# Kernel tuning notes

Measured on AMD Instinct MI355X. Metric: run time of the kernel, lower is better.

## Reference

```python
import jax, jax.numpy as jnp
import numpy as np

N_NODES = 100000
N_EDGES = 1600000
IN_DIM = 256
OUT_DIM = 128


def setup_inputs() -> dict:
    key = jax.random.key(0)
    k1, k2, k3, k4 = jax.random.split(key, 4)
    x = jax.random.normal(k1, (N_NODES, IN_DIM), dtype=jnp.float32)
    edge_list = jax.random.randint(k2, (2, N_EDGES), 0, N_NODES, dtype=jnp.int64)
    # xavier_uniform with gain=1.414
    gW = 1.414 * np.sqrt(6.0 / (IN_DIM + OUT_DIM))
    W = jax.random.uniform(k3, (IN_DIM, OUT_DIM), dtype=jnp.float32, minval=-gW, maxval=gW)
    ga = 1.414 * np.sqrt(6.0 / (2 * OUT_DIM + 1))
    a = jax.random.uniform(k4, (2 * OUT_DIM, 1), dtype=jnp.float32, minval=-ga, maxval=ga)
    return {"x": x, "edge_list": edge_list, "W": W, "a": a}


def reference(x, edge_list, W, a):
    N = x.shape[0]
    src, dst = edge_list[0], edge_list[1]
    h = x @ W  # [N, out_dim]
    # cat([h[src], h[dst]]) @ a  ==  h[src] @ a[:d] + h[dst] @ a[d:]
    d = h.shape[1]
    s_src = (h @ a[:d]).ravel()  # [N]
    s_dst = (h @ a[d:]).ravel()  # [N]
    e = jax.nn.leaky_relu(s_src[src] + s_dst[dst], negative_slope=0.2)  # [E]
    # sparse softmax over rows (segments = src node)
    seg_max = jax.ops.segment_max(e, src, num_segments=N)  # [N]
    ex = jnp.exp(e - seg_max[src])  # [E]
    denom = jax.ops.segment_sum(ex, src, num_segments=N)  # [N]
    attn = ex / jnp.where(denom > 0, denom, 1.0)[src]  # [E]
    # sparse aggregate: h_prime[i] = sum_{edges (i,j)} attn_ij * h[j]
    h_prime = jax.ops.segment_sum(attn[:, None] * h[dst], src, num_segments=N)  # [N, d]
    return jax.nn.elu(h_prime)
```

## Files before the change

kernel.cpp:

```cpp
#include <hip/hip_runtime.h>
#include <hip/hip_bf16.h>
#include <cstdint>
#include <cstddef>

#define NN 100000
#define NE 1600000
#define KD 256
#define OD 128
#define NB 391
#define CAP 8192
#define PCAP 9984
#define NGB 782

typedef __attribute__((ext_vector_type(8))) __bf16 bf16x8;
typedef __attribute__((ext_vector_type(4))) float f32x4;
typedef __attribute__((ext_vector_type(8))) unsigned short ushort8;

static __device__ __forceinline__ unsigned short f2bf(float f) {
  return __builtin_bit_cast(unsigned short, (__bf16)f);
}

__global__ void prep_wt_k(const float* __restrict__ W, unsigned short* __restrict__ Wt,
                          int* __restrict__ bcur) {
  const int i = blockIdx.x * 256 + threadIdx.x;
  const int k = i >> 7;
  const int n = i & 127;
  Wt[n * KD + k] = f2bf(W[i]);
  if (i < NB) bcur[i] = i * CAP;
}

__global__ __launch_bounds__(512, 4) void fused_k(
    const float* __restrict__ x, const unsigned short* __restrict__ Wt,
    const float* __restrict__ a, unsigned short* __restrict__ h,
    float* __restrict__ ssrc, float* __restrict__ sdst,
    const int* __restrict__ el, int* __restrict__ bcur,
    unsigned* __restrict__ stage) {
  __shared__ alignas(16) char smem[65536];
  const int t = threadIdx.x;

  if (blockIdx.x < NGB) {
    unsigned short* Bl = (unsigned short*)smem;
    const int lane = t & 63;
    const int wave = t >> 6;
    const int col = lane & 15;
    const int kg = lane >> 4;
    const int m0 = blockIdx.x * 128 + wave * 16;
    const int arow = m0 + col;
    const bool rowok = arow < NN;
    const float* __restrict__ xrow = x + (size_t)arow * KD;

    float4 fa[16];
    const float4 z4 = make_float4(0.f, 0.f, 0.f, 0.f);
#pragma unroll
    for (int s = 0; s < 8; ++s) {
      const int kk = s * 32 + kg * 8;
      fa[s * 2]     = rowok ? *(const float4*)(xrow + kk)     : z4;
      fa[s * 2 + 1] = rowok ? *(const float4*)(xrow + kk + 4) : z4;
    }

#pragma unroll
    for (int it = 0; it < 8; ++it) {
      const int c = it * 512 + t;
      const int r = c >> 5;
      const int c16 = c & 31;
      const ushort8 v = *(const ushort8*)(Wt + r * 256 + c16 * 8);
      const int byt = (r * 512 + c16 * 16) ^ ((r & 7) << 4);
      *(ushort8*)((char*)Bl + byt) = v;
    }
    __syncthreads();

    f32x4 acc[8];
#pragma unroll
    for (int i = 0; i < 8; ++i) acc[i] = (f32x4)0.0f;

#pragma unroll
    for (int s = 0; s < 8; ++s) {
      const float4 f0 = fa[s * 2];
      const float4 f1 = fa[s * 2 + 1];
      bf16x8 af;
      af[0] = (__bf16)f0.x; af[1] = (__bf16)f0.y; af[2] = (__bf16)f0.z; af[3] = (__bf16)f0.w;
      af[4] = (__bf16)f1.x; af[5] = (__bf16)f1.y; af[6] = (__bf16)f1.z; af[7] = (__bf16)f1.w;
#pragma unroll
      for (int nt = 0; nt < 8; ++nt) {
        const int n = nt * 16 + col;
        const int byt = (n * 512 + s * 64 + kg * 16) ^ ((col & 7) << 4);
        const ushort8 bu = *(const ushort8*)((const char*)Bl + byt);
        const bf16x8 bf = __builtin_bit_cast(bf16x8, bu);
        acc[nt] = __builtin_amdgcn_mfma_f32_16x16x32_bf16(af, bf, acc[nt], 0, 0, 0);
      }
    }

    float ps[4] = {0.f, 0.f, 0.f, 0.f};
    float pd[4] = {0.f, 0.f, 0.f, 0.f};
#pragma unroll
    for (int nt = 0; nt < 8; ++nt) {
      const int n = nt * 16 + col;
      const float av = a[n];
      const float av2 = a[OD + n];
#pragma unroll
      for (int r = 0; r < 4; ++r) {
        const float v = acc[nt][r];
        const int row = m0 + kg * 4 + r;
        if (row < NN) h[(size_t)row * OD + n] = f2bf(v);
        ps[r] += v * av;
        pd[r] += v * av2;
      }
    }
#pragma unroll
    for (int off = 1; off < 16; off <<= 1) {
#pragma unroll
      for (int r = 0; r < 4; ++r) {
        ps[r] += __shfl_xor(ps[r], off, 64);
        pd[r] += __shfl_xor(pd[r], off, 64);
      }
    }
    if (col == 0) {
#pragma unroll
      for (int r = 0; r < 4; ++r) {
        const int row = m0 + kg * 4 + r;
        if (row < NN) {
          ssrc[row] = ps[r] * 1.442695041f;
          sdst[row] = pd[r] * 1.442695041f;
        }
      }
    }
  } else {
    unsigned* sorted = (unsigned*)smem;
    unsigned short* bkid = (unsigned short*)(smem + 16384);
    int* hist  = (int*)(smem + 24576);
    int* off   = (int*)(smem + 26144);
    int* cur   = (int*)(smem + 27712);
    int* delta = (int*)(smem + 29276);
    const int te = (blockIdx.x - NGB) * 4096 + t * 8;
    int s[8], d[8];
    bool valid[8];
#pragma unroll
    for (int u = 0; u < 8; ++u) valid[u] = (te + u) < NE;
    if (te + 7 < NE) {
      const int4 a0 = *(const int4*)(el + te);
      const int4 a1 = *(const int4*)(el + te + 4);
      const int4 b0 = *(const int4*)(el + NE + te);
      const int4 b1 = *(const int4*)(el + NE + te + 4);
      s[0] = a0.x; s[1] = a0.y; s[2] = a0.z; s[3] = a0.w;
      s[4] = a1.x; s[5] = a1.y; s[6] = a1.z; s[7] = a1.w;
      d[0] = b0.x; d[1] = b0.y; d[2] = b0.z; d[3] = b0.w;
      d[4] = b1.x; d[5] = b1.y; d[6] = b1.z; d[7] = b1.w;
    } else {
#pragma unroll
      for (int u = 0; u < 8; ++u) {
        s[u] = valid[u] ? el[te + u] : 0;
        d[u] = valid[u] ? el[NE + te + u] : 0;
      }
    }
    for (int i = t; i <= NB; i += 512) hist[i] = 0;
    __syncthreads();
#pragma unroll
    for (int u = 0; u < 8; ++u)
      if (valid[u]) atomicAdd(&hist[s[u] >> 8], 1);
    __syncthreads();
    if (t < 64) {
      int v[7];
      int sum = 0;
#pragma unroll
      for (int i = 0; i < 7; ++i) {
        const int idx = t * 7 + i;
        v[i] = (idx <= NB) ? hist[idx] : 0;
        sum += v[i];
      }
      int pre = sum;
#pragma unroll
      for (int o = 1; o < 64; o <<= 1) {
        const int nb = __shfl_up(pre, o, 64);
        if (t >= o) pre += nb;
      }
      pre -= sum;
      int run = pre;
#pragma unroll
      for (int i = 0; i < 7; ++i) {
        const int idx = t * 7 + i;
        if (idx <= NB) off[idx] = run;
        run += v[i];
      }
    }
    __syncthreads();
    for (int i = t; i < NB; i += 512) cur[i] = off[i];
    __syncthreads();
#pragma unroll
    for (int u = 0; u < 8; ++u)
      if (valid[u]) {
        const int b = s[u] >> 8;
        const int p = atomicAdd(&cur[b], 1);
        sorted[p] = ((unsigned)(s[u] & 255) << 17) | (unsigned)d[u];
        bkid[p] = (unsigned short)b;
      }
    __syncthreads();
    for (int b = t; b < NB; b += 512) {
      const int len = off[b + 1] - off[b];
      if (len > 0) {
        const int gb = atomicAdd(&bcur[b], len);
        delta[b] = gb - off[b];
      }
    }
    __syncthreads();
    const int n = off[NB];
    for (int i = t; i < n; i += 512) {
      const int b = bkid[i];
      const int pos = delta[b] + i;
      if (pos < (b + 1) * CAP) stage[pos] = sorted[i];
    }
  }
}

__global__ __launch_bounds__(256) void place2_k(const unsigned* __restrict__ stage,
                                                const int* __restrict__ bcur,
                                                const float* __restrict__ ssrc,
                                                const float* __restrict__ sdst,
                                                unsigned* __restrict__ csrw,
                                                uint2* __restrict__ rc) {
  __shared__ unsigned ebuf[CAP];
  __shared__ float sl[256];
  __shared__ int hist2[256];
  __shared__ int exc[256];
  __shared__ int cur2[256];
  __shared__ unsigned firstd[256];
  const int b = blockIdx.x;
  const int t = threadIdx.x;
  const int node = b * 256 + t;
  const int base = b * PCAP;
  int tot = bcur[b] - b * CAP;
  tot = tot > CAP ? CAP : tot;
  hist2[t] = 0;
  sl[t] = (node < NN) ? ssrc[node] : 0.f;
  for (int i = t; i < tot; i += 256) ebuf[i] = stage[(size_t)b * CAP + i];
  __syncthreads();
  for (int i = t; i < tot; i += 256) atomicAdd(&hist2[ebuf[i] >> 17], 1);
  __syncthreads();
  if (t < 64) {
    int p[4];
    int sum = 0;
#pragma unroll
    for (int i = 0; i < 4; ++i) {
      const int c = hist2[t * 4 + i];
      p[i] = (c + 7) & ~7;
      sum += p[i];
    }
    int pre = sum;
#pragma unroll
    for (int o = 1; o < 64; o <<= 1) {
      const int nb = __shfl_up(pre, o, 64);
      if (t >= o) pre += nb;
    }
    pre -= sum;
    int run = pre;
#pragma unroll
    for (int i = 0; i < 4; ++i) { exc[t * 4 + i] = run; run += p[i]; }
  }
  __syncthreads();
  const int c = hist2[t];
  const int pc = (c + 7) & ~7;
  if (node < NN) rc[node] = make_uint2((unsigned)pc, (unsigned)(base + exc[t]));
  cur2[t] = exc[t];
  __syncthreads();
  for (int i = t; i < tot; i += 256) {
    const unsigned u = ebuf[i];
    const int s = u >> 17;
    const unsigned d = u & 0x1ffffu;
    const float sv = sl[s] + sdst[d];
    const float w = exp2f(fmaxf(sv, 0.2f * sv));
    unsigned wb = __builtin_bit_cast(unsigned, w);
    wb += 0x7fffu + ((wb >> 16) & 1u);
    const unsigned ent = ((wb >> 16) << 17) | d;
    const int p = atomicAdd(&cur2[s], 1);
    if (p == exc[s]) firstd[s] = d;
    csrw[base + p] = ent;
  }
  __syncthreads();
  if (c > 0) {
    const unsigned padent = firstd[t];
    const int e0 = exc[t];
    for (int i = c; i < pc; ++i) csrw[base + e0 + i] = padent;
  }
}

__global__ __launch_bounds__(256) void aggr_k(
    const unsigned short* __restrict__ h, const unsigned* __restrict__ csrw,
    const uint2* __restrict__ rc, float* __restrict__ out) {
  const int lane = threadIdx.x & 63;
  const int g = lane >> 4;
  const int sub = lane & 15;
  const int node = blockIdx.x * 4 + (threadIdx.x >> 6);
  const uint2 rcv = rc[node];
  const int pdeg = (int)rcv.x;
  const int r0 = (int)rcv.y;
  const uint4* __restrict__ hp = (const uint4*)h;
  float acc[8] = {0.f, 0.f, 0.f, 0.f, 0.f, 0.f, 0.f, 0.f};
  float sw = 0.f;
  const unsigned losel = 0x05040100u;
  const unsigned hisel = 0x07060302u;
  const unsigned onepk = 0x3F803F80u;
  const int nit = pdeg >> 3;
  if (nit > 0) {
    int j = r0 + g;
    unsigned uA0 = csrw[j];
    unsigned uA1 = csrw[j + 4];
    uint4 pA0 = hp[(uA0 & 0x1ffffu) * 16u + sub];
    uint4 pA1 = hp[(uA1 & 0x1ffffu) * 16u + sub];
    for (int it = 0; it < nit; ++it) {
      unsigned uB0, uB1;
      uint4 pB0, pB1;
      const bool more = (it + 1) < nit;
      if (more) {
        j += 8;
        uB0 = csrw[j];
        uB1 = csrw[j + 4];
        pB0 = hp[(uB0 & 0x1ffffu) * 16u + sub];
        pB1 = hp[(uB1 & 0x1ffffu) * 16u + sub];
      }
      const unsigned wpk = (uA0 >> 17) | ((uA1 >> 17) << 16);
      asm("v_dot2_f32_bf16 %0, %1, %2, %0" : "+v"(sw) : "v"(wpk), "v"(onepk));
      const unsigned k0a[4] = {pA0.x, pA0.y, pA0.z, pA0.w};
      const unsigned k1a[4] = {pA1.x, pA1.y, pA1.z, pA1.w};
#pragma unroll
      for (int q = 0; q < 4; ++q) {
        const unsigned lo = __builtin_amdgcn_perm(k1a[q], k0a[q], losel);
        const unsigned hi = __builtin_amdgcn_perm(k1a[q], k0a[q], hisel);
        asm("v_dot2_f32_bf16 %0, %1, %2, %0" : "+v"(acc[q * 2]) : "v"(wpk), "v"(lo));
        asm("v_dot2_f32_bf16 %0, %1, %2, %0" : "+v"(acc[q * 2 + 1]) : "v"(wpk), "v"(hi));
      }
      if (more) { uA0 = uB0; uA1 = uB1; pA0 = pB0; pA1 = pB1; }
    }
  }
#pragma unroll
  for (int off = 16; off < 64; off <<= 1) {
    sw += __shfl_xor(sw, off, 64);
#pragma unroll
    for (int q = 0; q < 8; ++q) acc[q] += __shfl_xor(acc[q], off, 64);
  }
  const float inv = pdeg > 0 ? 1.0f / sw : 0.f;
  float o[8];
#pragma unroll
  for (int q = 0; q < 8; ++q) {
    const float v = acc[q] * inv;
    o[q] = v > 0.f ? v : __expf(v) - 1.f;
  }
  if (lane < 16) {
    float4* op = (float4*)(out + (size_t)node * OD + sub * 8);
    op[0] = make_float4(o[0], o[1], o[2], o[3]);
    op[1] = make_float4(o[4], o[5], o[6], o[7]);
  }
}

extern "C" void kernel_launch(void* const* d_in, const int* in_sizes, int n_in,
                              void* d_out, int out_size, void* d_ws, size_t ws_size,
                              hipStream_t stream) {
  const float* x = (const float*)d_in[0];
  const int* el = (const int*)d_in[1];
  const float* W = (const float*)d_in[2];
  const float* a = (const float*)d_in[3];
  float* out = (float*)d_out;
  char* ws = (char*)d_ws;

  const size_t S = 400384;
  float* ssrc    = (float*)(ws + 0 * S);
  float* sdst    = (float*)(ws + 1 * S);
  uint2* rc      = (uint2*)(ws + 2 * S);
  int* bcur      = (int*)(ws + 4 * S);
  unsigned short* Wt = (unsigned short*)(ws + 4 * S + 8192);
  unsigned short* h  = (unsigned short*)(ws + 4 * S + 8192 + 65536);
  unsigned* csrw = (unsigned*)(ws + 4 * S + 8192 + 65536 + (size_t)NN * OD * 2);
  unsigned* stage = (unsigned*)d_out;

  prep_wt_k<<<128, 256, 0, stream>>>(W, Wt, bcur);
  fused_k<<<NGB + NB, 512, 0, stream>>>(x, Wt, a, h, ssrc, sdst, el, bcur, stage);
  place2_k<<<NB, 256, 0, stream>>>(stage, bcur, ssrc, sdst, csrw, rc);
  aggr_k<<<NN / 4, 256, 0, stream>>>(h, csrw, rc, out);
}
```

Measured before the change: 137.7 us.

## Batch up to five gather iterations in aggregation and relax fused kernel occupancy bound

The aggregation kernel now issues index loads for the first five 8-edge chunks, then all their row gathers, then computes, instead of a one-ahead software pipeline. The goal is more memory-level parallelism for typical degree-16 rows. Any remaining chunks fall back to a simple unpipelined loop. The fused GEMM/partition kernel's launch bound drops its min-blocks hint from 4 to 2, freeing registers at the possible cost of occupancy.

```diff
diff --git a/kernel.cpp b/kernel.cpp
--- a/kernel.cpp
+++ b/kernel.cpp
@@ -29,7 +29,7 @@
   if (i < NB) bcur[i] = i * CAP;
 }
 
-__global__ __launch_bounds__(512, 4) void fused_k(
+__global__ __launch_bounds__(512, 2) void fused_k(
     const float* __restrict__ x, const unsigned short* __restrict__ Wt,
     const float* __restrict__ a, unsigned short* __restrict__ h,
     float* __restrict__ ssrc, float* __restrict__ sdst,
@@ -299,27 +299,30 @@
   const unsigned hisel = 0x07060302u;
   const unsigned onepk = 0x3F803F80u;
   const int nit = pdeg >> 3;
-  if (nit > 0) {
-    int j = r0 + g;
-    unsigned uA0 = csrw[j];
-    unsigned uA1 = csrw[j + 4];
-    uint4 pA0 = hp[(uA0 & 0x1ffffu) * 16u + sub];
-    uint4 pA1 = hp[(uA1 & 0x1ffffu) * 16u + sub];
-    for (int it = 0; it < nit; ++it) {
-      unsigned uB0, uB1;
-      uint4 pB0, pB1;
-      const bool more = (it + 1) < nit;
-      if (more) {
-        j += 8;
-        uB0 = csrw[j];
-        uB1 = csrw[j + 4];
-        pB0 = hp[(uB0 & 0x1ffffu) * 16u + sub];
-        pB1 = hp[(uB1 & 0x1ffffu) * 16u + sub];
-      }
-      const unsigned wpk = (uA0 >> 17) | ((uA1 >> 17) << 16);
+  const int nit0 = nit > 5 ? 5 : nit;
+
+  unsigned ua[5], ub[5];
+  uint4 qa[5], qb[5];
+#pragma unroll
+  for (int s = 0; s < 5; ++s)
+    if (s < nit0) {
+      const int j = r0 + s * 8 + g;
+      ua[s] = csrw[j];
+      ub[s] = csrw[j + 4];
+    }
+#pragma unroll
+  for (int s = 0; s < 5; ++s)
+    if (s < nit0) {
+      qa[s] = hp[(ua[s] & 0x1ffffu) * 16u + sub];
+      qb[s] = hp[(ub[s] & 0x1ffffu) * 16u + sub];
+    }
+#pragma unroll
+  for (int s = 0; s < 5; ++s)
+    if (s < nit0) {
+      const unsigned wpk = (ua[s] >> 17) | ((ub[s] >> 17) << 16);
       asm("v_dot2_f32_bf16 %0, %1, %2, %0" : "+v"(sw) : "v"(wpk), "v"(onepk));
-      const unsigned k0a[4] = {pA0.x, pA0.y, pA0.z, pA0.w};
-      const unsigned k1a[4] = {pA1.x, pA1.y, pA1.z, pA1.w};
+      const unsigned k0a[4] = {qa[s].x, qa[s].y, qa[s].z, qa[s].w};
+      const unsigned k1a[4] = {qb[s].x, qb[s].y, qb[s].z, qb[s].w};
 #pragma unroll
       for (int q = 0; q < 4; ++q) {
         const unsigned lo = __builtin_amdgcn_perm(k1a[q], k0a[q], losel);
@@ -327,7 +330,23 @@
         asm("v_dot2_f32_bf16 %0, %1, %2, %0" : "+v"(acc[q * 2]) : "v"(wpk), "v"(lo));
         asm("v_dot2_f32_bf16 %0, %1, %2, %0" : "+v"(acc[q * 2 + 1]) : "v"(wpk), "v"(hi));
       }
-      if (more) { uA0 = uB0; uA1 = uB1; pA0 = pB0; pA1 = pB1; }
+    }
+  for (int it = 5; it < nit; ++it) {
+    const int j = r0 + it * 8 + g;
+    const unsigned u0 = csrw[j];
+    const unsigned u1 = csrw[j + 4];
+    const uint4 p0 = hp[(u0 & 0x1ffffu) * 16u + sub];
+    const uint4 p1 = hp[(u1 & 0x1ffffu) * 16u + sub];
+    const unsigned wpk = (u0 >> 17) | ((u1 >> 17) << 16);
+    asm("v_dot2_f32_bf16 %0, %1, %2, %0" : "+v"(sw) : "v"(wpk), "v"(onepk));
+    const unsigned k0a[4] = {p0.x, p0.y, p0.z, p0.w};
+    const unsigned k1a[4] = {p1.x, p1.y, p1.z, p1.w};
+#pragma unroll
+    for (int q = 0; q < 4; ++q) {
+      const unsigned lo = __builtin_amdgcn_perm(k1a[q], k0a[q], losel);
+      const unsigned hi = __builtin_amdgcn_perm(k1a[q], k0a[q], hisel);
+      asm("v_dot2_f32_bf16 %0, %1, %2, %0" : "+v"(acc[q * 2]) : "v"(wpk), "v"(lo));
+      asm("v_dot2_f32_bf16 %0, %1, %2, %0" : "+v"(acc[q * 2 + 1]) : "v"(wpk), "v"(hi));
     }
   }
 #pragma unroll
```

Result: no change. 139.1 us (+1.0%).
